# Optimization experiments

Hardware: AMD Instinct MI355X
Metric: run time of the kernel (lower is better)

The kernel has to match this reference:

```python
import jax, jax.numpy as jnp
import numpy as np

N_NODE = 100000
EMB = 128
N_EDGES = 1600000
LAYERS = 2
EPS = 1e-12  # torch F.normalize default eps


def setup_inputs() -> dict:
    key = jax.random.key(0)
    k1, k2, k3, k4, k5, k6 = jax.random.split(key, 6)
    return {
        "user_emb_weight": jax.random.normal(k1, (N_NODE, EMB), jnp.float32) * 0.02,
        "gate_w": jax.random.normal(k2, (EMB, EMB), jnp.float32) * (1.0 / np.sqrt(EMB)),
        "gate_b": jax.random.normal(k3, (EMB,), jnp.float32) * 0.01,
        "edge_rows": jax.random.randint(k4, (N_EDGES,), 0, N_NODE, jnp.int32),
        "edge_cols": jax.random.randint(k5, (N_EDGES,), 0, N_NODE, jnp.int32),
        "edge_vals": jax.random.uniform(k6, (N_EDGES,), jnp.float32),
        "layers": LAYERS,
    }


def _spmm(rows, cols, vals, x, n):
    # sparse [n,n] @ dense [n,d]: out[r] += v * x[c]
    gathered = vals[:, None] * x[cols]          # [nnz, d]
    return jax.ops.segment_sum(gathered, rows, num_segments=n)


def _l2_normalize(x):
    norm = jnp.sqrt(jnp.sum(x * x, axis=1, keepdims=True))
    return x / jnp.maximum(norm, EPS)


def reference(user_emb_weight, gate_w, gate_b, edge_rows, edge_cols, edge_vals, layers):
    n = user_emb_weight.shape[0]
    # self_gating: em * sigmoid(em @ W + b)
    u = user_emb_weight * jax.nn.sigmoid(user_emb_weight @ gate_w + gate_b)
    acc = u
    for _ in range(layers):
        u = _spmm(edge_rows, edge_cols, edge_vals, u, n)
        acc = acc + _l2_normalize(u)
    return acc
```

## Files before the change

### kernel.cpp

```cpp
#include <hip/hip_runtime.h>


typedef short s16x8 __attribute__((ext_vector_type(8)));
typedef float f32x4 __attribute__((ext_vector_type(4)));
typedef float f32x2 __attribute__((ext_vector_type(2)));

__device__ __forceinline__ float bflo(unsigned u) {
    union { unsigned u; float f; } x; x.u = u << 16; return x.f;
}
__device__ __forceinline__ float bfhi(unsigned u) {
    union { unsigned u; float f; } x; x.u = u & 0xffff0000u; return x.f;
}
__device__ __forceinline__ float bf1(unsigned short s) {
    union { unsigned u; float f; } x; x.u = (unsigned)s << 16; return x.f;
}
__device__ __forceinline__ unsigned short f2bf(float f) {
    union { float f; unsigned u; } x; x.f = f;
    unsigned r = x.u + 0x7fffu + ((x.u >> 16) & 1u);
    return (unsigned short)(r >> 16);
}
__device__ __forceinline__ unsigned pack2(float a, float b) {
    return (unsigned)f2bf(a) | ((unsigned)f2bf(b) << 16);
}
__device__ __forceinline__ float i2f(int i) {
    union { int i; float f; } x; x.i = i; return x.f;
}
__device__ __forceinline__ int f2i(float f) {
    union { float f; int i; } x; x.f = f; return x.i;
}
__device__ __forceinline__ f32x2 unpk(unsigned u) {
    union { unsigned u; float f; } lo, hi;
    lo.u = u << 16; hi.u = u & 0xffff0000u;
    f32x2 p; p.x = lo.f; p.y = hi.f; return p;
}

__global__ void detect_kernel(const unsigned* __restrict__ em, int nwords,
                              int* __restrict__ mode) {
    __shared__ int bad_s;
    if (threadIdx.x == 0) bad_s = 0;
    __syncthreads();
    int bad = 0;
    for (int i = threadIdx.x; i < nwords; i += blockDim.x) {
        unsigned u = em[i];
        unsigned e0 = (u >> 7) & 0xFFu;
        unsigned e1 = (u >> 23) & 0xFFu;
        if (e0 >= 157u || e1 >= 157u) bad = 1;
    }
    if (bad) atomicOr(&bad_s, 1);
    __syncthreads();
    if (threadIdx.x == 0) mode[0] = bad_s;
}

__global__ __launch_bounds__(256) void gating_mfma_kernel(
    const void* __restrict__ emv, const void* __restrict__ Wv,
    const void* __restrict__ bv,
    unsigned short* __restrict__ u_out,
    const int* __restrict__ mode_p, int n)
{
    __shared__ __align__(16) unsigned short Wt[128 * 136];
    const int fp32 = mode_p[0];
    const int tid = threadIdx.x;

    if (fp32) {
        const float* W = (const float*)Wv;
        for (int i = tid; i < 16384; i += 256) {
            int k = i >> 7, c = i & 127;
            Wt[c * 136 + k] = f2bf(W[i]);
        }
    } else {
        const unsigned short* W = (const unsigned short*)Wv;
        for (int i = tid; i < 16384; i += 256) {
            int k = i >> 7, c = i & 127;
            Wt[c * 136 + k] = W[i];
        }
    }
    __syncthreads();

    const int wave = tid >> 6, lane = tid & 63;
    const int quad = lane >> 4, l16 = lane & 15;

    s16x8 bfrag[8][4];
#pragma unroll
    for (int t = 0; t < 8; ++t)
#pragma unroll
        for (int kb = 0; kb < 4; ++kb) {
            int col = t * 16 + l16;
            int k = kb * 32 + quad * 8;
            bfrag[t][kb] = *(const s16x8*)&Wt[col * 136 + k];
        }

    float bias[8];
    if (fp32) {
        const float* b = (const float*)bv;
#pragma unroll
        for (int t = 0; t < 8; ++t) bias[t] = b[t * 16 + l16];
    } else {
        const unsigned short* b = (const unsigned short*)bv;
#pragma unroll
        for (int t = 0; t < 8; ++t) bias[t] = bf1(b[t * 16 + l16]);
    }

    const int nstrips = (n + 15) >> 4;
    const int gwaves = gridDim.x * 4;
    for (int s = blockIdx.x * 4 + wave; s < nstrips; s += gwaves) {
        const int m0 = s * 16;
        const int arow = m0 + l16;

        s16x8 afrag[4];
        if (fp32) {
            const float* em = (const float*)emv;
#pragma unroll
            for (int kb = 0; kb < 4; ++kb) {
                union { unsigned u[4]; s16x8 v; } cv;
                if (arow < n) {
                    const float* src = em + (size_t)arow * 128 + kb * 32 + quad * 8;
                    float4 f0 = *(const float4*)(src);
                    float4 f1 = *(const float4*)(src + 4);
                    cv.u[0] = pack2(f0.x, f0.y); cv.u[1] = pack2(f0.z, f0.w);
                    cv.u[2] = pack2(f1.x, f1.y); cv.u[3] = pack2(f1.z, f1.w);
                } else { cv.u[0] = cv.u[1] = cv.u[2] = cv.u[3] = 0; }
                afrag[kb] = cv.v;
            }
        } else {
            const unsigned short* em = (const unsigned short*)emv;
#pragma unroll
            for (int kb = 0; kb < 4; ++kb) {
                union { uint4 u; s16x8 v; } cv;
                if (arow < n)
                    cv.u = *(const uint4*)(em + (size_t)arow * 128 + kb * 32 + quad * 8);
                else
                    cv.u = make_uint4(0, 0, 0, 0);
                afrag[kb] = cv.v;
            }
        }

        f32x4 acc[8];
#pragma unroll
        for (int t = 0; t < 8; ++t) {
            f32x4 a = {0.f, 0.f, 0.f, 0.f};
#pragma unroll
            for (int kb = 0; kb < 4; ++kb)
                a = __builtin_amdgcn_mfma_f32_16x16x32_bf16(afrag[kb], bfrag[t][kb], a, 0, 0, 0);
            acc[t] = a;
        }

#pragma unroll
        for (int t = 0; t < 8; ++t) {
            const int col = t * 16 + l16;
#pragma unroll
            for (int r = 0; r < 4; ++r) {
                const int row = m0 + quad * 4 + r;
                if (row < n) {
                    float e;
                    if (fp32) e = ((const float*)emv)[(size_t)row * 128 + col];
                    else      e = bf1(((const unsigned short*)emv)[(size_t)row * 128 + col]);
                    float g = 1.f / (1.f + __expf(-(acc[t][r] + bias[t])));
                    u_out[(size_t)row * 128 + col] = f2bf(e * g);
                }
            }
        }
    }
}

#define CHUNK 4096
#define MAXE  5120

__global__ __launch_bounds__(256) void bucket_hist_kernel(
    const int* __restrict__ erow, int* __restrict__ bcnt, int nnz)
{
    __shared__ int l[512];
    int tid = threadIdx.x;
    l[tid] = 0; l[tid + 256] = 0;
    __syncthreads();
    int c0 = blockIdx.x * CHUNK;
    int cend = min(c0 + CHUNK, nnz);
    for (int i = c0 + tid; i < cend; i += 256)
        atomicAdd(&l[(unsigned)erow[i] >> 8], 1);
    __syncthreads();
    if (l[tid]) atomicAdd(&bcnt[tid], l[tid]);
    if (l[tid + 256]) atomicAdd(&bcnt[tid + 256], l[tid + 256]);
}

__global__ __launch_bounds__(256) void bucket_scan_kernel(
    const int* __restrict__ bcnt, int* __restrict__ bbase,
    int* __restrict__ gcursor, int* __restrict__ rp, int n, int B, int nnz)
{
    __shared__ int s[512], tsum[256];
    int tid = threadIdx.x;
    s[tid] = (tid < B) ? bcnt[tid] : 0;
    s[tid + 256] = (tid + 256 < B) ? bcnt[tid + 256] : 0;
    __syncthreads();
    int a0 = s[2 * tid], a1 = s[2 * tid + 1];
    tsum[tid] = a0 + a1;
    __syncthreads();
#pragma unroll
    for (int off = 1; off < 256; off <<= 1) {
        int t = (tid >= off) ? tsum[tid - off] : 0;
        __syncthreads();
        tsum[tid] += t;
        __syncthreads();
    }
    int excl = (tid == 0) ? 0 : tsum[tid - 1];
    if (2 * tid < B)     { bbase[2 * tid] = excl;          gcursor[2 * tid] = excl; }
    if (2 * tid + 1 < B) { bbase[2 * tid + 1] = excl + a0; gcursor[2 * tid + 1] = excl + a0; }
    if (tid == 0) { bbase[B] = nnz; rp[n] = nnz; }
}

__global__ __launch_bounds__(256) void partition_kernel(
    const int* __restrict__ erow, const int* __restrict__ ecol,
    const void* __restrict__ eval, int* __restrict__ gcursor,
    int2* __restrict__ sev_tmp, const int* __restrict__ mode_p, int nnz)
{
    __shared__ int lcnt[512], lbase[512];
    int tid = threadIdx.x;
    lcnt[tid] = 0; lcnt[tid + 256] = 0;
    __syncthreads();
    int c0 = blockIdx.x * CHUNK;
    int cend = min(c0 + CHUNK, nnz);
    for (int i = c0 + tid; i < cend; i += 256)
        atomicAdd(&lcnt[(unsigned)erow[i] >> 8], 1);
    __syncthreads();
    int c256 = lcnt[tid], c512 = lcnt[tid + 256];
    if (c256 > 0) lbase[tid] = atomicAdd(&gcursor[tid], c256);
    if (c512 > 0) lbase[tid + 256] = atomicAdd(&gcursor[tid + 256], c512);
    __syncthreads();
    lcnt[tid] = 0; lcnt[tid + 256] = 0;
    __syncthreads();
    const int fp32 = mode_p[0];
    for (int i = c0 + tid; i < cend; i += 256) {
        int row = erow[i];
        int bkt = (unsigned)row >> 8;
        int rank = atomicAdd(&lcnt[bkt], 1);
        float v = fp32 ? ((const float*)eval)[i]
                       : bf1(((const unsigned short*)eval)[i]);
        int x = ((row & 255) << 17) | ecol[i];
        sev_tmp[lbase[bkt] + rank] = make_int2(x, f2i(v));
    }
}

__global__ __launch_bounds__(256) void csr_fin_kernel(
    const int* __restrict__ bbase, const int2* __restrict__ sev_tmp,
    int2* __restrict__ sev, int* __restrict__ rp, int n)
{
    __shared__ int2 ev[MAXE];
    __shared__ int rcnt[256], tsum[256];
    int b = blockIdx.x;
    int base = bbase[b];
    int size = bbase[b + 1] - base;
    int tid = threadIdx.x;
    rcnt[tid] = 0;
    __syncthreads();
    bool fits = (size <= MAXE);
    if (fits) {
        for (int e = tid; e < size; e += 256) {
            int2 t = sev_tmp[base + e];
            ev[e] = t;
            atomicAdd(&rcnt[(unsigned)t.x >> 17], 1);
        }
    } else {
        for (int e = tid; e < size; e += 256)
            atomicAdd(&rcnt[(unsigned)sev_tmp[base + e].x >> 17], 1);
    }
    __syncthreads();
    int myc = rcnt[tid];
    tsum[tid] = myc;
    __syncthreads();
#pragma unroll
    for (int off = 1; off < 256; off <<= 1) {
        int t = (tid >= off) ? tsum[tid - off] : 0;
        __syncthreads();
        tsum[tid] += t;
        __syncthreads();
    }
    int excl = tsum[tid] - myc;
    int row0 = b << 8;
    if (row0 + tid < n) rp[row0 + tid] = base + excl;
    __syncthreads();
    rcnt[tid] = excl;
    __syncthreads();
    for (int e = tid; e < size; e += 256) {
        int2 t = fits ? ev[e] : sev_tmp[base + e];
        int r = (unsigned)t.x >> 17;
        int k = atomicAdd(&rcnt[r], 1);
        sev[base + k] = make_int2(t.x & 0x1FFFF, t.y);
    }
}

__global__ __launch_bounds__(256) void spmm_norm_kernel(
    const int* __restrict__ rp, const int2* __restrict__ sev,
    const uint4* __restrict__ u_in, uint4* __restrict__ u_out,
    float* __restrict__ scale_out,
    const uint4* __restrict__ g_in, const uint4* __restrict__ prev_u,
    const float* __restrict__ prev_scale,
    void* __restrict__ out, const int* __restrict__ mode_p, int n)
{
    int w = (int)((blockIdx.x * (unsigned)blockDim.x + threadIdx.x) >> 6);
    int lane = threadIdx.x & 63;
    if (w >= n) return;
    const int q = lane >> 4, l16 = lane & 15;
    int e0 = rp[w], e1 = rp[w + 1];
    f32x2 a0 = {0.f, 0.f}, a1 = {0.f, 0.f}, a2 = {0.f, 0.f}, a3 = {0.f, 0.f};

    for (int e = e0; e < e1; e += 16) {
        const int last = e1 - 1;
        const int i0 = e + q, i1 = e + 4 + q, i2 = e + 8 + q, i3 = e + 12 + q;
        int2 m0 = sev[min(i0, last)];
        int2 m1 = sev[min(i1, last)];
        int2 m2 = sev[min(i2, last)];
        int2 m3 = sev[min(i3, last)];
        uint4 g0 = u_in[(unsigned)(m0.x << 4) + l16];
        uint4 g1 = u_in[(unsigned)(m1.x << 4) + l16];
        uint4 g2 = u_in[(unsigned)(m2.x << 4) + l16];
        uint4 g3 = u_in[(unsigned)(m3.x << 4) + l16];
        float v0 = (i0 < e1) ? i2f(m0.y) : 0.f;
        float v1 = (i1 < e1) ? i2f(m1.y) : 0.f;
        float v2 = (i2 < e1) ? i2f(m2.y) : 0.f;
        float v3 = (i3 < e1) ? i2f(m3.y) : 0.f;
        f32x2 vv0 = {v0, v0}, vv1 = {v1, v1}, vv2 = {v2, v2}, vv3 = {v3, v3};
        a0 = __builtin_elementwise_fma(vv0, unpk(g0.x), a0);
        a1 = __builtin_elementwise_fma(vv0, unpk(g0.y), a1);
        a2 = __builtin_elementwise_fma(vv0, unpk(g0.z), a2);
        a3 = __builtin_elementwise_fma(vv0, unpk(g0.w), a3);
        a0 = __builtin_elementwise_fma(vv1, unpk(g1.x), a0);
        a1 = __builtin_elementwise_fma(vv1, unpk(g1.y), a1);
        a2 = __builtin_elementwise_fma(vv1, unpk(g1.z), a2);
        a3 = __builtin_elementwise_fma(vv1, unpk(g1.w), a3);
        a0 = __builtin_elementwise_fma(vv2, unpk(g2.x), a0);
        a1 = __builtin_elementwise_fma(vv2, unpk(g2.y), a1);
        a2 = __builtin_elementwise_fma(vv2, unpk(g2.z), a2);
        a3 = __builtin_elementwise_fma(vv2, unpk(g2.w), a3);
        a0 = __builtin_elementwise_fma(vv3, unpk(g3.x), a0);
        a1 = __builtin_elementwise_fma(vv3, unpk(g3.y), a1);
        a2 = __builtin_elementwise_fma(vv3, unpk(g3.z), a2);
        a3 = __builtin_elementwise_fma(vv3, unpk(g3.w), a3);
    }

    float a[8] = {a0.x, a0.y, a1.x, a1.y, a2.x, a2.y, a3.x, a3.y};

#pragma unroll
    for (int j = 0; j < 8; ++j) {
        a[j] += __shfl_xor(a[j], 16, 64);
        a[j] += __shfl_xor(a[j], 32, 64);
    }
    float s = 0.f;
#pragma unroll
    for (int j = 0; j < 8; ++j) s = fmaf(a[j], a[j], s);
#pragma unroll
    for (int off = 8; off > 0; off >>= 1) s += __shfl_xor(s, off, 64);
    float scale = 1.f / fmaxf(sqrtf(s), 1e-12f);

    if (q == 0 && u_out) {
        uint4 o;
        o.x = pack2(a[0], a[1]); o.y = pack2(a[2], a[3]);
        o.z = pack2(a[4], a[5]); o.w = pack2(a[6], a[7]);
        u_out[(size_t)w * 16 + l16] = o;
    }
    if (lane == 0 && scale_out) scale_out[w] = scale;

    if (q == 1 && prev_u) {
        float s1 = prev_scale[w];
        uint4 gv = g_in[(size_t)w * 16 + l16];
        uint4 p1 = prev_u[(size_t)w * 16 + l16];
        float r0 = bflo(gv.x) + bflo(p1.x) * s1 + a[0] * scale;
        float r1 = bfhi(gv.x) + bfhi(p1.x) * s1 + a[1] * scale;
        float r2 = bflo(gv.y) + bflo(p1.y) * s1 + a[2] * scale;
        float r3 = bfhi(gv.y) + bfhi(p1.y) * s1 + a[3] * scale;
        float r4 = bflo(gv.z) + bflo(p1.z) * s1 + a[4] * scale;
        float r5 = bfhi(gv.z) + bfhi(p1.z) * s1 + a[5] * scale;
        float r6 = bflo(gv.w) + bflo(p1.w) * s1 + a[6] * scale;
        float r7 = bfhi(gv.w) + bfhi(p1.w) * s1 + a[7] * scale;
        if (mode_p[0]) {
            float* ap = (float*)out + (size_t)w * 128 + l16 * 8;
            float4 c0, c1;
            c0.x = r0; c0.y = r1; c0.z = r2; c0.w = r3;
            c1.x = r4; c1.y = r5; c1.z = r6; c1.w = r7;
            *(float4*)ap = c0; *(float4*)(ap + 4) = c1;
        } else {
            uint4 o;
            o.x = pack2(r0, r1); o.y = pack2(r2, r3);
            o.z = pack2(r4, r5); o.w = pack2(r6, r7);
            ((uint4*)out)[(size_t)w * 16 + l16] = o;
        }
    }
}

extern "C" void kernel_launch(void* const* d_in, const int* in_sizes, int n_in,
                              void* d_out, int out_size, void* d_ws, size_t ws_size,
                              hipStream_t stream)
{
    const void* em   = d_in[0];
    const void* gw   = d_in[1];
    const void* gb   = d_in[2];
    const int*  erow = (const int*)d_in[3];
    const int*  ecol = (const int*)d_in[4];
    const void* eval = d_in[5];

    int n   = in_sizes[0] / 128;
    int nnz = in_sizes[3];
    int B   = (n + 255) >> 8;
    int nblk_e = (nnz + CHUNK - 1) / CHUNK;

    char* ws = (char*)d_ws;
    size_t off = 0;
    auto carve = [&](size_t bytes) -> void* {
        void* p = ws + off;
        off += (bytes + 255) & ~(size_t)255;
        return p;
    };
    size_t nd = (size_t)n * 128;
    int*      mode    = (int*)carve(4);
    unsigned* uA      = (unsigned*)carve(nd * 2);
    unsigned* uB      = (unsigned*)carve(nd * 2);
    int*      rp      = (int*)carve((size_t)(n + 1) * 4);
    float*    scale1  = (float*)carve((size_t)n * 4);
    int*      bcnt    = (int*)carve(512 * 4);
    int*      bbase   = (int*)carve(516 * 4);
    int*      gcursor = (int*)carve(512 * 4);
    int2*     sev     = (int2*)carve((size_t)nnz * 8);
    int2*     sev_tmp = (int2*)uB;

    hipMemsetAsync(bcnt, 0, 512 * 4, stream);
    detect_kernel<<<1, 256, 0, stream>>>((const unsigned*)em, 8192, mode);

    gating_mfma_kernel<<<512, 256, 0, stream>>>(em, gw, gb, (unsigned short*)uA, mode, n);
    bucket_hist_kernel<<<nblk_e, 256, 0, stream>>>(erow, bcnt, nnz);
    bucket_scan_kernel<<<1, 256, 0, stream>>>(bcnt, bbase, gcursor, rp, n, B, nnz);
    partition_kernel<<<nblk_e, 256, 0, stream>>>(erow, ecol, eval, gcursor, sev_tmp, mode, nnz);
    csr_fin_kernel<<<B, 256, 0, stream>>>(bbase, sev_tmp, sev, rp, n);

    spmm_norm_kernel<<<(n + 3) / 4, 256, 0, stream>>>(
        rp, sev, (const uint4*)uA, (uint4*)uB, scale1,
        nullptr, nullptr, nullptr, nullptr, mode, n);
    spmm_norm_kernel<<<(n + 3) / 4, 256, 0, stream>>>(
        rp, sev, (const uint4*)uB, nullptr, nullptr,
        (const uint4*)uA, (const uint4*)uB, scale1, d_out, mode, n);
}
```

Measured before the change: 346.7 us.

## Map one row per 16-lane quarter-wave in SpMM instead of one row per wavefront

Each wavefront now handles four rows, one per 16-lane group, instead of splitting one row's edges across four quarter-waves. This drops the cross-quarter shuffle reduction and uses the whole wave when rows have few edges (average degree about 16). The loop runs until the longest of the four rows is done, so lanes on shorter rows sit idle under degree imbalance. The launch uses a quarter as many blocks.

```diff
diff --git a/kernel.cpp b/kernel.cpp
--- a/kernel.cpp
+++ b/kernel.cpp
@@ -294,16 +294,26 @@
     const float* __restrict__ prev_scale,
     void* __restrict__ out, const int* __restrict__ mode_p, int n)
 {
-    int w = (int)((blockIdx.x * (unsigned)blockDim.x + threadIdx.x) >> 6);
-    int lane = threadIdx.x & 63;
-    if (w >= n) return;
+    const int wv = (int)((blockIdx.x * (unsigned)blockDim.x + threadIdx.x) >> 6);
+    const int lane = threadIdx.x & 63;
     const int q = lane >> 4, l16 = lane & 15;
-    int e0 = rp[w], e1 = rp[w + 1];
+    const int row = wv * 4 + q;
+    const bool rowok = row < n;
+    const int rsafe = rowok ? row : (n - 1);
+
+    int e0 = rp[rsafe];
+    int e1 = rowok ? rp[rsafe + 1] : e0;
+    const int d = e1 - e0;
+    int dm = max(d, __shfl_xor(d, 16, 64));
+    dm = max(dm, __shfl_xor(dm, 32, 64));
+    const int iters = (dm + 3) >> 2;
+    const int last = max(e1 - 1, 0);
+
     f32x2 a0 = {0.f, 0.f}, a1 = {0.f, 0.f}, a2 = {0.f, 0.f}, a3 = {0.f, 0.f};
 
-    for (int e = e0; e < e1; e += 16) {
-        const int last = e1 - 1;
-        const int i0 = e + q, i1 = e + 4 + q, i2 = e + 8 + q, i3 = e + 12 + q;
+    for (int t = 0; t < iters; ++t) {
+        const int base = e0 + t * 4;
+        const int i0 = base, i1 = base + 1, i2 = base + 2, i3 = base + 3;
         int2 m0 = sev[min(i0, last)];
         int2 m1 = sev[min(i1, last)];
         int2 m2 = sev[min(i2, last)];
@@ -337,11 +347,6 @@
 
     float a[8] = {a0.x, a0.y, a1.x, a1.y, a2.x, a2.y, a3.x, a3.y};
 
-#pragma unroll
-    for (int j = 0; j < 8; ++j) {
-        a[j] += __shfl_xor(a[j], 16, 64);
-        a[j] += __shfl_xor(a[j], 32, 64);
-    }
     float s = 0.f;
 #pragma unroll
     for (int j = 0; j < 8; ++j) s = fmaf(a[j], a[j], s);
@@ -349,37 +354,39 @@
     for (int off = 8; off > 0; off >>= 1) s += __shfl_xor(s, off, 64);
     float scale = 1.f / fmaxf(sqrtf(s), 1e-12f);
 
-    if (q == 0 && u_out) {
-        uint4 o;
-        o.x = pack2(a[0], a[1]); o.y = pack2(a[2], a[3]);
-        o.z = pack2(a[4], a[5]); o.w = pack2(a[6], a[7]);
-        u_out[(size_t)w * 16 + l16] = o;
-    }
-    if (lane == 0 && scale_out) scale_out[w] = scale;
-
-    if (q == 1 && prev_u) {
-        float s1 = prev_scale[w];
-        uint4 gv = g_in[(size_t)w * 16 + l16];
-        uint4 p1 = prev_u[(size_t)w * 16 + l16];
-        float r0 = bflo(gv.x) + bflo(p1.x) * s1 + a[0] * scale;
-        float r1 = bfhi(gv.x) + bfhi(p1.x) * s1 + a[1] * scale;
-        float r2 = bflo(gv.y) + bflo(p1.y) * s1 + a[2] * scale;
-        float r3 = bfhi(gv.y) + bfhi(p1.y) * s1 + a[3] * scale;
-        float r4 = bflo(gv.z) + bflo(p1.z) * s1 + a[4] * scale;
-        float r5 = bfhi(gv.z) + bfhi(p1.z) * s1 + a[5] * scale;
-        float r6 = bflo(gv.w) + bflo(p1.w) * s1 + a[6] * scale;
-        float r7 = bfhi(gv.w) + bfhi(p1.w) * s1 + a[7] * scale;
-        if (mode_p[0]) {
-            float* ap = (float*)out + (size_t)w * 128 + l16 * 8;
-            float4 c0, c1;
-            c0.x = r0; c0.y = r1; c0.z = r2; c0.w = r3;
-            c1.x = r4; c1.y = r5; c1.z = r6; c1.w = r7;
-            *(float4*)ap = c0; *(float4*)(ap + 4) = c1;
-        } else {
+    if (rowok) {
+        if (u_out) {
             uint4 o;
-            o.x = pack2(r0, r1); o.y = pack2(r2, r3);
-            o.z = pack2(r4, r5); o.w = pack2(r6, r7);
-            ((uint4*)out)[(size_t)w * 16 + l16] = o;
+            o.x = pack2(a[0], a[1]); o.y = pack2(a[2], a[3]);
+            o.z = pack2(a[4], a[5]); o.w = pack2(a[6], a[7]);
+            u_out[(size_t)row * 16 + l16] = o;
+        }
+        if (l16 == 0 && scale_out) scale_out[row] = scale;
+
+        if (prev_u) {
+            float s1 = prev_scale[row];
+            uint4 gv = g_in[(size_t)row * 16 + l16];
+            uint4 p1 = prev_u[(size_t)row * 16 + l16];
+            float r0 = bflo(gv.x) + bflo(p1.x) * s1 + a[0] * scale;
+            float r1 = bfhi(gv.x) + bfhi(p1.x) * s1 + a[1] * scale;
+            float r2 = bflo(gv.y) + bflo(p1.y) * s1 + a[2] * scale;
+            float r3 = bfhi(gv.y) + bfhi(p1.y) * s1 + a[3] * scale;
+            float r4 = bflo(gv.z) + bflo(p1.z) * s1 + a[4] * scale;
+            float r5 = bfhi(gv.z) + bfhi(p1.z) * s1 + a[5] * scale;
+            float r6 = bflo(gv.w) + bflo(p1.w) * s1 + a[6] * scale;
+            float r7 = bfhi(gv.w) + bfhi(p1.w) * s1 + a[7] * scale;
+            if (mode_p[0]) {
+                float* ap = (float*)out + (size_t)row * 128 + l16 * 8;
+                float4 c0, c1;
+                c0.x = r0; c0.y = r1; c0.z = r2; c0.w = r3;
+                c1.x = r4; c1.y = r5; c1.z = r6; c1.w = r7;
+                *(float4*)ap = c0; *(float4*)(ap + 4) = c1;
+            } else {
+                uint4 o;
+                o.x = pack2(r0, r1); o.y = pack2(r2, r3);
+                o.z = pack2(r4, r5); o.w = pack2(r6, r7);
+                ((uint4*)out)[(size_t)row * 16 + l16] = o;
+            }
         }
     }
 }
@@ -428,10 +435,11 @@
     partition_kernel<<<nblk_e, 256, 0, stream>>>(erow, ecol, eval, gcursor, sev_tmp, mode, nnz);
     csr_fin_kernel<<<B, 256, 0, stream>>>(bbase, sev_tmp, sev, rp, n);
 
-    spmm_norm_kernel<<<(n + 3) / 4, 256, 0, stream>>>(
+    int nblk_s = (n + 15) / 16;
+    spmm_norm_kernel<<<nblk_s, 256, 0, stream>>>(
         rp, sev, (const uint4*)uA, (uint4*)uB, scale1,
         nullptr, nullptr, nullptr, nullptr, mode, n);
-    spmm_norm_kernel<<<(n + 3) / 4, 256, 0, stream>>>(
+    spmm_norm_kernel<<<nblk_s, 256, 0, stream>>>(
         rp, sev, (const uint4*)uB, nullptr, nullptr,
         (const uint4*)uA, (const uint4*)uB, scale1, d_out, mode, n);
 }
```

Result: no change. 346.2 us (-0.2%).
